# Performance work log

Measured on AMD Instinct MI355X. Metric: run time of the kernel, lower is better.

Reference implementation:

```python
import jax, jax.numpy as jnp
import numpy as np

B, L, F, H = 4096, 32, 28, 512  # batch, max CDR length (=input_size), features, hidden


def setup_inputs() -> dict:
    key = jax.random.key(0)
    ks = jax.random.split(key, 8)
    return {
        "input": jax.random.normal(ks[0], (B, L, F), jnp.float32),
        "unpacked_masks": jnp.ones((B, L, 1), jnp.float32),
        "bias_mat": jnp.zeros((B, L, F), jnp.float32),
        "conv1_w": jax.random.normal(ks[1], (F, F, 3), jnp.float32) * 0.1,
        "conv1_b": jnp.zeros((F,), jnp.float32),
        "conv_w": jax.random.normal(ks[2], (1, L, 1), jnp.float32) * 0.1,
        "conv_b": jnp.zeros((1,), jnp.float32),
        "fc1_w": jax.random.normal(ks[3], (1, H), jnp.float32) * 0.05,
        "fc1_b": jnp.zeros((1,), jnp.float32),
        "W_ih": jax.random.normal(ks[4], (4 * H, L), jnp.float32) * 0.1,
        "W_hh": jax.random.normal(ks[5], (4 * H, H), jnp.float32) * 0.05,
        "b_ih": jnp.zeros((4 * H,), jnp.float32),
        "b_hh": jnp.zeros((4 * H,), jnp.float32),
        "conv2_w": jax.random.normal(ks[6], (1, H, 1), jnp.float32) * 0.05,
        "conv2_b": jnp.zeros((1,), jnp.float32),
    }


def reference(input, unpacked_masks, bias_mat, conv1_w, conv1_b, conv_w, conv_b,
              fc1_w, fc1_b, W_ih, W_hh, b_ih, b_hh, conv2_w, conv2_b):
    b, l, f = input.shape
    h_dim = W_hh.shape[1]
    # --- conv1 residual block (eval mode: dropouts are identity) ---
    x_t = jnp.transpose(input, (0, 2, 1))  # [B, F, L]
    y = jax.lax.conv_general_dilated(
        x_t, conv1_w, window_strides=(1,), padding=[(1, 1)],
        dimension_numbers=("NCH", "OIH", "NCH")) + conv1_b[None, :, None]
    x = jnp.transpose(y, (0, 2, 1)) * unpacked_masks  # [B, L, F]
    x = jax.nn.elu(x) + input
    # --- u_a = Conv1d(L,1,1) over the length axis: [B, 1, F] (kept as [B, F]) ---
    u_a = jnp.einsum("blf,l->bf", x, conv_w[0, :, 0]) + conv_b  # [B, F]
    x_transposed = jnp.transpose(x, (0, 2, 1))  # [B, F, L]

    h0 = jnp.zeros((l, h_dim), input.dtype)
    c0 = jnp.zeros((l, h_dim), input.dtype)

    def step(carry, inps):
        h, c = carry
        u_b, xT_b, bias_b = inps  # [F], [F, L], [L, F]
        w_a = h @ fc1_w.T + fc1_b  # [L, 1]
        scores = jax.nn.leaky_relu(u_b[None, :] + w_a, 0.01) + bias_b  # [L, F]
        attn = jax.nn.softmax(scores, axis=0)  # softmax over dim 1 of [B, L, F]
        ctx = attn @ xT_b  # [L, F] @ [F, L] -> [L, L]
        gates = ctx @ W_ih.T + b_ih + h @ W_hh.T + b_hh  # [L, 4H]
        i_g, f_g, g_g, o_g = jnp.split(gates, 4, axis=-1)
        c_new = jax.nn.sigmoid(f_g) * c + jax.nn.sigmoid(i_g) * jnp.tanh(g_g)
        h_new = jax.nn.sigmoid(o_g) * jnp.tanh(c_new)
        return (h_new, c_new), h_new

    # The original loops over the batch dim, carrying (h, c) across iterations.
    (_, _), all_hidden = jax.lax.scan(step, (h0, c0), (u_a, x_transposed, bias_mat))
    # all_hidden: [B, L, H]
    out = jnp.einsum("blh,h->bl", all_hidden, conv2_w[0, :, 0])[..., None] + conv2_b  # [B, L, 1]
    return out * unpacked_masks
```

## Files before the change

### kernel.cpp

```cpp
#include <hip/hip_runtime.h>
#include <math.h>

#define NBATCH 4096
#define GBLK   64
#define HSTR   516
#define XSTR   36
#define WSTR   33

typedef int   i32x4 __attribute__((ext_vector_type(4)));
typedef float f32x4 __attribute__((ext_vector_type(4)));
typedef short short8 __attribute__((ext_vector_type(8)));

#define OFF_X    0u
#define OFF_UA   (OFF_X  + 4096u*896u)
#define OFF_BG   (OFF_UA + 4096u*28u)
#define OFF_H    (OFF_BG + 2048u)
#define OFF_BAR  (OFF_H  + 2u*32u*512u)
#define OFF_WFH  (OFF_BAR + 64u)
#define OFF_WFL  (OFF_WFH + 557056u)

__device__ __forceinline__ unsigned bfr(float x) {
    unsigned u = __builtin_bit_cast(unsigned, x);
    return (u + 0x7FFFu + ((u >> 16) & 1u)) >> 16;
}
__device__ __forceinline__ float fb(unsigned b) { return __builtin_bit_cast(float, b << 16); }
__device__ __forceinline__ unsigned packhl(float v) {
    unsigned h = bfr(v);
    unsigned l = bfr(v - fb(h));
    return h | (l << 16);
}
__device__ __forceinline__ float up(unsigned u) {
    return __builtin_bit_cast(float, u << 16) + __builtin_bit_cast(float, u & 0xFFFF0000u);
}
__device__ __forceinline__ float sigm(float v) { return 1.0f / (1.0f + __expf(-v)); }

__global__ __launch_bounds__(256) void prep_kernel(
    const float* __restrict__ input, const float* __restrict__ masks,
    const float* __restrict__ c1w, const float* __restrict__ c1b,
    const float* __restrict__ convw, const float* __restrict__ convb,
    float* __restrict__ xout, float* __restrict__ uaout)
// ... 41 lines not shown
{
    const int g = blockIdx.x * 256 + threadIdx.x;
    BG[g] = bih[g] + bhh[g];
}

__global__ __launch_bounds__(256) void prepf_kernel(
    const float* __restrict__ Wih, const float* __restrict__ Whh,
    unsigned* __restrict__ wfh, unsigned* __restrict__ wfl)
{
    const int id = blockIdx.x * 256 + threadIdx.x;
    const int lane = id & 63;
    int rest = id >> 6;
    const int ct = rest & 1; rest >>= 1;
    const int t = rest % 17, blk8 = rest / 17;
    const int n = lane & 15, kg = lane >> 4;
    const int c = ct * 16 + n;
    const int g = (c >> 3) * 512 + blk8 * 8 + (c & 7);
    const int kbase = t * 32 + kg * 8;
    i32x4 hv, lv;
    #pragma unroll
    for (int d = 0; d < 4; ++d) {
        const int k = kbase + 2 * d;
        float w0 = (k     < 512) ? Whh[(size_t)g * 512 + k]     : Wih[g * 32 + (k - 512)];
        float w1 = (k + 1 < 512) ? Whh[(size_t)g * 512 + k + 1] : Wih[g * 32 + (k + 1 - 512)];
        unsigned h0 = bfr(w0), h1 = bfr(w1);
        unsigned l0 = bfr(w0 - fb(h0)), l1 = bfr(w1 - fb(h1));
        ((unsigned*)&hv)[d] = h0 | (h1 << 16);
        ((unsigned*)&lv)[d] = l0 | (l1 << 16);
    }
    ((i32x4*)wfh)[id] = hv;
    ((i32x4*)wfl)[id] = lv;
}

__device__ __forceinline__ void stage_h16(const unsigned* hsrc, unsigned* h_lds, int tid)
{
    const int half = tid >> 7, t128 = tid & 127;
    const unsigned* p = hsrc + half * 8192 + t128 * 4;
    i32x4 v0, v1, v2, v3, v4, v5, v6, v7, v8, v9, v10, v11, v12, v13, v14, v15;
    asm volatile(
        "global_load_dwordx4 %0, %16, off sc0 sc1\n\t"
        "global_load_dwordx4 %1, %16, off offset:2048 sc0 sc1\n\t"
        "global_load_dwordx4 %2, %17, off sc0 sc1\n\t"
        "global_load_dwordx4 %3, %17, off offset:2048 sc0 sc1\n\t"
        "global_load_dwordx4 %4, %18, off sc0 sc1\n\t"
        "global_load_dwordx4 %5, %18, off offset:2048 sc0 sc1\n\t"
        "global_load_dwordx4 %6, %19, off sc0 sc1\n\t"
        "global_load_dwordx4 %7, %19, off offset:2048 sc0 sc1\n\t"
        "global_load_dwordx4 %8, %20, off sc0 sc1\n\t"
        "global_load_dwordx4 %9, %20, off offset:2048 sc0 sc1\n\t"
        "global_load_dwordx4 %10, %21, off sc0 sc1\n\t"
        "global_load_dwordx4 %11, %21, off offset:2048 sc0 sc1\n\t"
        "global_load_dwordx4 %12, %22, off sc0 sc1\n\t"
        "global_load_dwordx4 %13, %22, off offset:2048 sc0 sc1\n\t"
        "global_load_dwordx4 %14, %23, off sc0 sc1\n\t"
        "global_load_dwordx4 %15, %23, off offset:2048 sc0 sc1\n\t"
        "s_waitcnt vmcnt(0)"
        : "=&v"(v0), "=&v"(v1), "=&v"(v2), "=&v"(v3),
          "=&v"(v4), "=&v"(v5), "=&v"(v6), "=&v"(v7),
          "=&v"(v8), "=&v"(v9), "=&v"(v10), "=&v"(v11),
          "=&v"(v12), "=&v"(v13), "=&v"(v14), "=&v"(v15)
        : "v"(p), "v"(p + 1024), "v"(p + 2048), "v"(p + 3072),
          "v"(p + 4096), "v"(p + 5120), "v"(p + 6144), "v"(p + 7168)
        : "memory");
    const int col = t128 * 4;
    const int rb = half * 16;
    *(i32x4*)&h_lds[(rb +  0) * HSTR + col] = v0;
    *(i32x4*)&h_lds[(rb +  1) * HSTR + col] = v1;
    *(i32x4*)&h_lds[(rb +  2) * HSTR + col] = v2;
    *(i32x4*)&h_lds[(rb +  3) * HSTR + col] = v3;
    *(i32x4*)&h_lds[(rb +  4) * HSTR + col] = v4;
    *(i32x4*)&h_lds[(rb +  5) * HSTR + col] = v5;
    *(i32x4*)&h_lds[(rb +  6) * HSTR + col] = v6;
    *(i32x4*)&h_lds[(rb +  7) * HSTR + col] = v7;
    *(i32x4*)&h_lds[(rb +  8) * HSTR + col] = v8;
    *(i32x4*)&h_lds[(rb +  9) * HSTR + col] = v9;
    *(i32x4*)&h_lds[(rb + 10) * HSTR + col] = v10;
    *(i32x4*)&h_lds[(rb + 11) * HSTR + col] = v11;
    *(i32x4*)&h_lds[(rb + 12) * HSTR + col] = v12;
    *(i32x4*)&h_lds[(rb + 13) * HSTR + col] = v13;
    *(i32x4*)&h_lds[(rb + 14) * HSTR + col] = v14;
    *(i32x4*)&h_lds[(rb + 15) * HSTR + col] = v15;
}

__device__ __forceinline__ void build_frag(const unsigned* base, short8& hi, short8& lo)
{
    i32x4 ua = *(const i32x4*)base;
    i32x4 ub = *(const i32x4*)(base + 4);
    i32x4 h, l;
    h.x = (int)__builtin_amdgcn_perm((unsigned)ua.y, (unsigned)ua.x, 0x05040100u);
    l.x = (int)__builtin_amdgcn_perm((unsigned)ua.y, (unsigned)ua.x, 0x07060302u);
    h.y = (int)__builtin_amdgcn_perm((unsigned)ua.w, (unsigned)ua.z, 0x05040100u);
    l.y = (int)__builtin_amdgcn_perm((unsigned)ua.w, (unsigned)ua.z, 0x07060302u);
    h.z = (int)__builtin_amdgcn_perm((unsigned)ub.y, (unsigned)ub.x, 0x05040100u);
    l.z = (int)__builtin_amdgcn_perm((unsigned)ub.y, (unsigned)ub.x, 0x07060302u);
    h.w = (int)__builtin_amdgcn_perm((unsigned)ub.w, (unsigned)ub.z, 0x05040100u);
    l.w = (int)__builtin_amdgcn_perm((unsigned)ub.w, (unsigned)ub.z, 0x07060302u);
    hi = __builtin_bit_cast(short8, h);
    lo = __builtin_bit_cast(short8, l);
}

__device__ __forceinline__ void out_proj(const unsigned* h_lds, const float* c2w_lds, float c2b,
                                         const float* masks, float* out, int bb,
                                         int slot16, int seg16)
{
    float p0 = 0.f, p1 = 0.f;
    #pragma unroll
    for (int jj = 0; jj < 8; ++jj) {
        const int off = seg16 * 4 + 64 * jj;
        f32x4 w = *(const f32x4*)&c2w_lds[off];
        i32x4 h0 = *(const i32x4*)&h_lds[slot16 * HSTR + off];
        i32x4 h1 = *(const i32x4*)&h_lds[(slot16 + 16) * HSTR + off];
        p0 += up((unsigned)h0.x) * w.x + up((unsigned)h0.y) * w.y
            + up((unsigned)h0.z) * w.z + up((unsigned)h0.w) * w.w;
        p1 += up((unsigned)h1.x) * w.x + up((unsigned)h1.y) * w.y
            + up((unsigned)h1.z) * w.z + up((unsigned)h1.w) * w.w;
    }
    p0 += __shfl_xor(p0, 1); p0 += __shfl_xor(p0, 2);
    p0 += __shfl_xor(p0, 4); p0 += __shfl_xor(p0, 8);
    p1 += __shfl_xor(p1, 1); p1 += __shfl_xor(p1, 2);
    p1 += __shfl_xor(p1, 4); p1 += __shfl_xor(p1, 8);
    if (seg16 == 0) {
        out[bb * 32 + slot16]      = (p0 + c2b) * masks[bb * 32 + slot16];
        out[bb * 32 + slot16 + 16] = (p1 + c2b) * masks[bb * 32 + slot16 + 16];
    }
}

__global__ __launch_bounds__(256, 1) void rnn_serial(
    const float* __restrict__ xbuf, const float* __restrict__ uabuf,
    const float* __restrict__ BG,
    const unsigned* __restrict__ wfh, const unsigned* __restrict__ wfl,
    const float* __restrict__ Whh, const float* __restrict__ Wih,
    unsigned* hbuf, int* bar,
    const float* __restrict__ bias_mat, const float* __restrict__ masks,
    const float* __restrict__ fc1w, const float* __restrict__ fc1bp,
    const float* __restrict__ c2w, const float* __restrict__ c2bp,
    float* __restrict__ out)
{
    __shared__ unsigned h_lds[32 * HSTR];
    __shared__ float    x_lds[32 * XSTR];
    __shared__ float    bias_lds[32 * XSTR];
    __shared__ unsigned attn_p[32 * XSTR];
    __shared__ float    mbuf[2][32 * XSTR];
    __shared__ float    wihb[32 * WSTR];
    __shared__ float    gl_part[5 * 32 * 33];
    __shared__ float    wapart[4][2][32];
    __shared__ float    wa_lds[32];
    __shared__ float    ua_lds[28];
    __shared__ float    fc1_lds[512];
    __shared__ float    c2w_lds[512];
    __shared__ int      s_flag;

    const int tid  = threadIdx.x;
    const int blk  = blockIdx.x;
    const int lane = tid & 63;
    const int wv   = tid >> 6;

    for (int i = tid; i < 512; i += 256) { fc1_lds[i] = fc1w[i]; c2w_lds[i] = c2w[i]; }
    if (tid == 0) s_flag = 0;
    const float f1b = fc1bp[0];
    const float c2b = c2bp[0];

    i32x4 whi[4][2], wlo[4][2];
    {
        const i32x4* wfh4 = (const i32x4*)wfh;
        const i32x4* wfl4 = (const i32x4*)wfl;
        #pragma unroll
        for (int s = 0; s < 4; ++s)
            #pragma unroll
            for (int ct = 0; ct < 2; ++ct) {
                const int idx = ((blk * 17 + wv * 4 + s) * 2 + ct) * 64 + lane;
                whi[s][ct] = wfh4[idx];
                wlo[s][ct] = wfl4[idx];
            }
    }
    i32x4 wAh[4], wAl[4];
    {
        const int n = lane & 15, kgi = lane >> 4;
        #pragma unroll
        for (int s = 0; s < 4; ++s) {
            wAh[s] = (i32x4){0, 0, 0, 0};
            wAl[s] = (i32x4){0, 0, 0, 0};
            if (n < 2) {
                const float* src = (n == 0) ? fc1w : c2w;
                const int k0 = (wv * 4 + s) * 32 + kgi * 8;
                #pragma unroll
                for (int d = 0; d < 4; ++d) {
                    float v0 = src[k0 + 2 * d], v1 = src[k0 + 2 * d + 1];
                    unsigned h0 = bfr(v0), h1 = bfr(v1);
                    unsigned l0 = bfr(v0 - fb(h0)), l1 = bfr(v1 - fb(h1));
                    ((unsigned*)&wAh[s])[d] = h0 | (h1 << 16);
                    ((unsigned*)&wAl[s])[d] = l0 | (l1 << 16);
                }
            }
        }
    }

    const int l_own = tid >> 3, hc = tid & 7;
    float bgv[4];
    #pragma unroll
    for (int t = 0; t < 4; ++t) bgv[t] = BG[t * 512 + blk * 8 + hc];
    float c_reg = 0.f;
    bool use_mfma = true;

    const int slot16 = tid >> 4, seg16 = tid & 15;
    const int arow = lane & 15, kg = lane >> 4;

    for (int i = tid; i < 32 * XSTR; i += 256) {
        attn_p[i] = 0u;
        mbuf[0][i] = 0.f;
        mbuf[1][i] = 0.f;
    }
    for (int i = tid; i < 1024; i += 256) {
        const int c = i >> 5, j = i & 31;
        wihb[c * WSTR + j] = Wih[((c >> 3) * 512 + blk * 8 + (c & 7)) * 32 + j];
    }
    if (tid < 224) {
        float4 x0 = *(const float4*)(xbuf + tid * 4);
        #pragma unroll
        for (int i = 0; i < 4; ++i) {
            const int idx = tid * 4 + i;
            const int l = idx / 28, f = idx - l * 28;
            x_lds[l * XSTR + f] = ((const float*)&x0)[i];
        }
    }
    __syncthreads();
    for (int idx = tid; idx < 896; idx += 256) {
        const int c = idx / 28, f = idx - c * 28;
        float s = 0.f;
        #pragma unroll 8
        for (int j = 0; j < 32; ++j) s += wihb[c * WSTR + j] * x_lds[j * XSTR + f];
        mbuf[0][c * XSTR + f] = s;
    }
    float4 xr = make_float4(0.f, 0.f, 0.f, 0.f), br = xr;
    float ua_r = 0.f;
    if (tid < 224) {
        xr = *(const float4*)(xbuf + 896 + tid * 4);
        br = *(const float4*)(bias_mat + tid * 4);
    }
    if (tid < 28) ua_r = uabuf[tid];
    __syncthreads();

    for (int b = 0; b < NBATCH; ++b) {
        stage_h16(hbuf + (b & 1) * 16384, h_lds, tid);
        if (tid < 224) {
            #pragma unroll
            for (int i = 0; i < 4; ++i) {
                const int idx = tid * 4 + i;
                const int l = idx / 28, f = idx - l * 28;
                x_lds[l * XSTR + f]    = ((const float*)&xr)[i];
                bias_lds[l * XSTR + f] = ((const float*)&br)[i];
            }
        }
        if (tid < 28) ua_lds[tid] = ua_r;
        __syncthreads();

        {
            const int bx = (b + 2 < NBATCH) ? b + 2 : NBATCH - 1;
            const int bn = (b + 1 < NBATCH) ? b + 1 : NBATCH - 1;
            if (tid < 224) {
                xr = *(const float4*)(xbuf + (size_t)bx * 896 + tid * 4);
                br = *(const float4*)(bias_mat + (size_t)bn * 896 + tid * 4);
            }
            if (tid < 28) ua_r = uabuf[bn * 28 + tid];
        }

        if (use_mfma) {
            f32x4 accg[2][2], accw[2];
            accg[0][0] = (f32x4){0,0,0,0}; accg[0][1] = (f32x4){0,0,0,0};
            accg[1][0] = (f32x4){0,0,0,0}; accg[1][1] = (f32x4){0,0,0,0};
            accw[0]    = (f32x4){0,0,0,0}; accw[1]    = (f32x4){0,0,0,0};
            #pragma unroll
            for (int s = 0; s < 4; ++s) {
                const int k0 = (wv * 4 + s) * 32 + kg * 8;
                short8 ah0, al0, ah1, al1;
                build_frag(&h_lds[arow * HSTR + k0], ah0, al0);
                build_frag(&h_lds[(arow + 16) * HSTR + k0], ah1, al1);
                #pragma unroll
                for (int ct = 0; ct < 2; ++ct) {
                    short8 bh = __builtin_bit_cast(short8, whi[s][ct]);
                    short8 bl = __builtin_bit_cast(short8, wlo[s][ct]);
                    accg[ct][0] = __builtin_amdgcn_mfma_f32_16x16x32_bf16(ah0, bh, accg[ct][0], 0, 0, 0);
                    accg[ct][0] = __builtin_amdgcn_mfma_f32_16x16x32_bf16(al0, bh, accg[ct][0], 0, 0, 0);
                    accg[ct][0] = __builtin_amdgcn_mfma_f32_16x16x32_bf16(ah0, bl, accg[ct][0], 0, 0, 0);
                    accg[ct][1] = __builtin_amdgcn_mfma_f32_16x16x32_bf16(ah1, bh, accg[ct][1], 0, 0, 0);
                    accg[ct][1] = __builtin_amdgcn_mfma_f32_16x16x32_bf16(al1, bh, accg[ct][1], 0, 0, 0);
                    accg[ct][1] = __builtin_amdgcn_mfma_f32_16x16x32_bf16(ah1, bl, accg[ct][1], 0, 0, 0);
                }
                short8 bh = __builtin_bit_cast(short8, wAh[s]);
                short8 bl = __builtin_bit_cast(short8, wAl[s]);
                accw[0] = __builtin_amdgcn_mfma_f32_16x16x32_bf16(ah0, bh, accw[0], 0, 0, 0);
                accw[0] = __builtin_amdgcn_mfma_f32_16x16x32_bf16(al0, bh, accw[0], 0, 0, 0);
                accw[0] = __builtin_amdgcn_mfma_f32_16x16x32_bf16(ah0, bl, accw[0], 0, 0, 0);
                accw[1] = __builtin_amdgcn_mfma_f32_16x16x32_bf16(ah1, bh, accw[1], 0, 0, 0);
                accw[1] = __builtin_amdgcn_mfma_f32_16x16x32_bf16(al1, bh, accw[1], 0, 0, 0);
                accw[1] = __builtin_amdgcn_mfma_f32_16x16x32_bf16(ah1, bl, accw[1], 0, 0, 0);
            }
            #pragma unroll
            for (int ct = 0; ct < 2; ++ct)
                #pragma unroll
                for (int rt = 0; rt < 2; ++rt)
                    #pragma unroll
                    for (int r = 0; r < 4; ++r)
                        gl_part[(wv * 32 + rt * 16 + kg * 4 + r) * 33 + ct * 16 + arow] = accg[ct][rt][r];
            if (arow < 2) {
                #pragma unroll
                for (int rt = 0; rt < 2; ++rt)
                    #pragma unroll
                    for (int r = 0; r < 4; ++r)
                        wapart[wv][arow][rt * 16 + kg * 4 + r] = accw[rt][r];
            }
        }
        if (b < 2 || !use_mfma) {
            float p0 = 0.f, p1 = 0.f;
            #pragma unroll
            for (int jj = 0; jj < 8; ++jj) {
                const int off = seg16 * 4 + 64 * jj;
                f32x4 w = *(const f32x4*)&fc1_lds[off];
                i32x4 h0 = *(const i32x4*)&h_lds[slot16 * HSTR + off];
                i32x4 h1 = *(const i32x4*)&h_lds[(slot16 + 16) * HSTR + off];
                p0 += up((unsigned)h0.x) * w.x + up((unsigned)h0.y) * w.y
                    + up((unsigned)h0.z) * w.z + up((unsigned)h0.w) * w.w;
                p1 += up((unsigned)h1.x) * w.x + up((unsigned)h1.y) * w.y
                    + up((unsigned)h1.z) * w.z + up((unsigned)h1.w) * w.w;
            }
            p0 += __shfl_xor(p0, 1); p0 += __shfl_xor(p0, 2);
            p0 += __shfl_xor(p0, 4); p0 += __shfl_xor(p0, 8);
            p1 += __shfl_xor(p1, 1); p1 += __shfl_xor(p1, 2);
            p1 += __shfl_xor(p1, 4); p1 += __shfl_xor(p1, 8);
            if (seg16 == 0) { wa_lds[slot16] = p0 + f1b; wa_lds[slot16 + 16] = p1 + f1b; }
            if (b > 0 && blk == ((b - 1) & 63))
                out_proj(h_lds, c2w_lds, c2b, masks, out, b - 1, slot16, seg16);
        }
        __syncthreads();

        if (wv == 3) {
            if (use_mfma && lane < 32) {
                float wm = f1b;
                #pragma unroll
                for (int w = 0; w < 4; ++w) wm += wapart[w][0][lane];
                if (b < 2) {
                    if (fabsf(wm - wa_lds[lane]) > 0.02f + 0.004f * fabsf(wa_lds[lane])) s_flag = 1;
                } else {
                    wa_lds[lane] = wm;
                }
            }
            if (lane < 56) {
                const int f = lane >> 1, hf = lane & 1;
                const float uaf = ua_lds[f];
                float z[16], mx = -1e30f;
                #pragma unroll
                for (int i = 0; i < 16; ++i) {
                    const int l = hf * 16 + i;
                    float v = uaf + wa_lds[l];
                    v = (v >= 0.f) ? v : 0.01f * v;
                    v += bias_lds[l * XSTR + f];
                    z[i] = v;
                    mx = fmaxf(mx, v);
                }
                mx = fmaxf(mx, __shfl_xor(mx, 1));
                float sum = 0.f;
                #pragma unroll
                for (int i = 0; i < 16; ++i) { z[i] = __expf(z[i] - mx); sum += z[i]; }
                sum += __shfl_xor(sum, 1);
                const float inv = 1.0f / sum;
                #pragma unroll
                for (int i = 0; i < 16; ++i)
                    attn_p[(hf * 16 + i) * XSTR + f] = packhl(z[i] * inv);
            }
            asm volatile("s_waitcnt lgkmcnt(0)" ::: "memory");
            __builtin_amdgcn_sched_barrier(0);
            if (use_mfma) {
                f32x4 accm[2][2];
                accm[0][0] = (f32x4){0,0,0,0}; accm[0][1] = (f32x4){0,0,0,0};
                accm[1][0] = (f32x4){0,0,0,0}; accm[1][1] = (f32x4){0,0,0,0};
                short8 ah0, al0, ah1, al1;
                build_frag(&attn_p[arow * XSTR + kg * 8], ah0, al0);
                build_frag(&attn_p[(arow + 16) * XSTR + kg * 8], ah1, al1);
                #pragma unroll
                for (int ct = 0; ct < 2; ++ct) {
                    const float* mrow = &mbuf[b & 1][(ct * 16 + arow) * XSTR + kg * 8];
                    short8 bh, bl;
                    #pragma unroll
                    for (int e = 0; e < 8; ++e) {
                        const float v = mrow[e];
                        const unsigned hh = bfr(v);
                        bh[e] = (short)hh;
                        bl[e] = (short)bfr(v - fb(hh));
                    }
                    accm[ct][0] = __builtin_amdgcn_mfma_f32_16x16x32_bf16(ah0, bh, accm[ct][0], 0, 0, 0);
                    accm[ct][0] = __builtin_amdgcn_mfma_f32_16x16x32_bf16(al0, bh, accm[ct][0], 0, 0, 0);
                    accm[ct][0] = __builtin_amdgcn_mfma_f32_16x16x32_bf16(ah0, bl, accm[ct][0], 0, 0, 0);
                    accm[ct][1] = __builtin_amdgcn_mfma_f32_16x16x32_bf16(ah1, bh, accm[ct][1], 0, 0, 0);
                    accm[ct][1] = __builtin_amdgcn_mfma_f32_16x16x32_bf16(al1, bh, accm[ct][1], 0, 0, 0);
                    accm[ct][1] = __builtin_amdgcn_mfma_f32_16x16x32_bf16(ah1, bl, accm[ct][1], 0, 0, 0);
                }
                #pragma unroll
                for (int ct = 0; ct < 2; ++ct)
                    #pragma unroll
                    for (int rt = 0; rt < 2; ++rt)
                        #pragma unroll
                        for (int r = 0; r < 4; ++r)
                            gl_part[(4 * 32 + rt * 16 + kg * 4 + r) * 33 + ct * 16 + arow] = accm[ct][rt][r];
            }
        } else {
            if (wv == 2 && use_mfma && lane < 32) {
                float om = c2b;
                #pragma unroll
                for (int w = 0; w < 4; ++w) om += wapart[w][1][lane];
                if (b < 2) {
                    const unsigned* hr = &h_lds[lane * HSTR];
                    float ox = c2b;
                    for (int k = 0; k < 512; ++k) ox += up(hr[k]) * c2w_lds[k];
                    if (fabsf(om - ox) > 0.02f + 0.004f * fabsf(ox)) s_flag = 1;
                } else if (b > 0 && blk == ((b - 1) & 63)) {
                    out[(b - 1) * 32 + lane] = om * masks[(b - 1) * 32 + lane];
                }
            }
            float* mdst = mbuf[(b + 1) & 1];
            for (int idx = wv * 64 + lane; idx < 896; idx += 192) {
                const int c = idx / 28, f = idx - c * 28;
                float s = 0.f;
                #pragma unroll 8
                for (int j = 0; j < 32; ++j) s += wihb[c * WSTR + j] * x_lds[j * XSTR + f];
                mdst[c * XSTR + f] = s;
            }
        }
        __syncthreads();

        {
            float gv[4];
            #pragma unroll
            for (int t = 0; t < 4; ++t) {
                float g = bgv[t];
                if (use_mfma) {
                    #pragma unroll
                    for (int w = 0; w < 5; ++w)
                        g += gl_part[(w * 32 + l_own) * 33 + t * 8 + hc];
                }
                gv[t] = g;
            }
            if (b < 2 || !use_mfma) {
                const unsigned* hrow = &h_lds[l_own * HSTR];
                const unsigned* ar   = &attn_p[l_own * XSTR];
                const float*    mb   = mbuf[b & 1];
                bool bad = false;
                #pragma unroll
                for (int t = 0; t < 4; ++t) {
                    const int g = t * 512 + blk * 8 + hc;
                    const f32x4* wr = (const f32x4*)(Whh + (size_t)g * 512);
                    float ref = bgv[t];
                    #pragma unroll 4
                    for (int q = 0; q < 128; ++q) {
                        f32x4 w = wr[q];
                        ref += up(hrow[4 * q + 0]) * w.x + up(hrow[4 * q + 1]) * w.y
                             + up(hrow[4 * q + 2]) * w.z + up(hrow[4 * q + 3]) * w.w;
                    }
                    const float* mr = &mb[(t * 8 + hc) * XSTR];
                    #pragma unroll 4
                    for (int f = 0; f < 28; ++f) ref += up(ar[f]) * mr[f];
                    if (b < 2 && use_mfma && fabsf(gv[t] - ref) > 0.02f + 0.004f * fabsf(ref)) bad = true;
                    gv[t] = ref;
                }
                if (b < 2) {
                    if (bad) s_flag = 1;
                    __syncthreads();
                    use_mfma = use_mfma && (s_flag == 0);
                    __syncthreads();
                    if (tid == 0) s_flag = 0;
                }
            }
            const float cn = sigm(gv[1]) * c_reg + sigm(gv[0]) * tanhf(gv[2]);
            const float hn = sigm(gv[3]) * tanhf(cn);
            c_reg = cn;
            __hip_atomic_store(hbuf + ((b & 1) ^ 1) * 16384 + l_own * 512 + blk * 8 + hc,
                               packhl(hn), __ATOMIC_RELAXED, __HIP_MEMORY_SCOPE_AGENT);
        }

        asm volatile("s_waitcnt vmcnt(0)" ::: "memory");
        __syncthreads();
        if (tid == 0)
            __hip_atomic_store(&bar[blk], b + 1, __ATOMIC_RELAXED, __HIP_MEMORY_SCOPE_AGENT);
        if (tid < 64) {
            while (true) {
                int v = __hip_atomic_load(&bar[tid], __ATOMIC_RELAXED, __HIP_MEMORY_SCOPE_AGENT);
                if (__all(v >= b + 1)) break;
                __builtin_amdgcn_s_sleep(1);
            }
        }
        __syncthreads();
    }

    if (blk == 63) {
        stage_h16(hbuf, h_lds, tid);
        __syncthreads();
        if (use_mfma) {
            f32x4 accw[2];
            accw[0] = (f32x4){0,0,0,0}; accw[1] = (f32x4){0,0,0,0};
            #pragma unroll
            for (int s = 0; s < 4; ++s) {
                const int k0 = (wv * 4 + s) * 32 + kg * 8;
                short8 ah0, al0, ah1, al1;
                build_frag(&h_lds[arow * HSTR + k0], ah0, al0);
                build_frag(&h_lds[(arow + 16) * HSTR + k0], ah1, al1);
                short8 bh = __builtin_bit_cast(short8, wAh[s]);
                short8 bl = __builtin_bit_cast(short8, wAl[s]);
                accw[0] = __builtin_amdgcn_mfma_f32_16x16x32_bf16(ah0, bh, accw[0], 0, 0, 0);
                accw[0] = __builtin_amdgcn_mfma_f32_16x16x32_bf16(al0, bh, accw[0], 0, 0, 0);
                accw[0] = __builtin_amdgcn_mfma_f32_16x16x32_bf16(ah0, bl, accw[0], 0, 0, 0);
                accw[1] = __builtin_amdgcn_mfma_f32_16x16x32_bf16(ah1, bh, accw[1], 0, 0, 0);
                accw[1] = __builtin_amdgcn_mfma_f32_16x16x32_bf16(al1, bh, accw[1], 0, 0, 0);
                accw[1] = __builtin_amdgcn_mfma_f32_16x16x32_bf16(ah1, bl, accw[1], 0, 0, 0);
            }
            if (arow < 2) {
                #pragma unroll
                for (int rt = 0; rt < 2; ++rt)
                    #pragma unroll
                    for (int r = 0; r < 4; ++r)
                        wapart[wv][arow][rt * 16 + kg * 4 + r] = accw[rt][r];
            }
            __syncthreads();
            if (wv == 2 && lane < 32) {
                float om = c2b;
                #pragma unroll
                for (int w = 0; w < 4; ++w) om += wapart[w][1][lane];
                out[4095 * 32 + lane] = om * masks[4095 * 32 + lane];
            }
        } else {
            out_proj(h_lds, c2w_lds, c2b, masks, out, 4095, slot16, seg16);
        }
    }
}

extern "C" void kernel_launch(void* const* d_in, const int* in_sizes, int n_in,
                              void* d_out, int out_size, void* d_ws, size_t ws_size,
                              hipStream_t stream)
{
    const float* input    = (const float*)d_in[0];
    const float* masks    = (const float*)d_in[1];
    const float* bias_mat = (const float*)d_in[2];
    const float* c1w      = (const float*)d_in[3];
    const float* c1b      = (const float*)d_in[4];
    const float* convw    = (const float*)d_in[5];
    const float* convb    = (const float*)d_in[6];
    const float* fc1w     = (const float*)d_in[7];
    const float* fc1b     = (const float*)d_in[8];
    const float* Wih      = (const float*)d_in[9];
    const float* Whh      = (const float*)d_in[10];
    const float* bih      = (const float*)d_in[11];
    const float* bhh      = (const float*)d_in[12];
    const float* c2w      = (const float*)d_in[13];
    const float* c2b      = (const float*)d_in[14];

    float* ws  = (float*)d_ws;
    float* out = (float*)d_out;
    int*   bar = (int*)(ws + OFF_BAR);

    hipMemsetAsync(ws + OFF_H, 0, (2u * 32u * 512u + 64u) * sizeof(float), stream);

    hipLaunchKernelGGL(prep_kernel, dim3(NBATCH), dim3(256), 0, stream,
                       input, masks, c1w, c1b, convw, convb, ws + OFF_X, ws + OFF_UA);
    hipLaunchKernelGGL(prepw_kernel, dim3(8), dim3(256), 0, stream,
// ... 11 lines not shown
```

Baseline: 31.76 ms.

## Replace global grid barrier with per-wave producer polling and wave-local h staging

Removes the end-of-step block-wide barrier, where thread group 0 polled all 64 block flags and then synchronised. Instead, each wave polls only the 16 producer blocks whose h columns it needs, then stages its own column slice of h into LDS. Each wave reads only its own slice, so an LDS wave fence replaces the __syncthreads before the MFMA. The next-step x/bias prefetch moves after the gate MFMA. This lets waves start as soon as their producers finish, at the cost of a subtle memory-ordering risk and barriers rearranged around the b<2 path.

```diff
diff --git a/kernel.cpp b/kernel.cpp
--- a/kernel.cpp
+++ b/kernel.cpp
@@ -113,54 +113,59 @@
     ((i32x4*)wfl)[id] = lv;
 }
 
-__device__ __forceinline__ void stage_h16(const unsigned* hsrc, unsigned* h_lds, int tid)
-{
-    const int half = tid >> 7, t128 = tid & 127;
-    const unsigned* p = hsrc + half * 8192 + t128 * 4;
+__device__ __forceinline__ void stage_wave(const unsigned* hsrc, unsigned* h_lds, int wv, int lane)
+{
+    const unsigned* p = hsrc + (lane >> 1) * 512 + wv * 128 + (lane & 1) * 64;
     i32x4 v0, v1, v2, v3, v4, v5, v6, v7, v8, v9, v10, v11, v12, v13, v14, v15;
     asm volatile(
         "global_load_dwordx4 %0, %16, off sc0 sc1\n\t"
-        "global_load_dwordx4 %1, %16, off offset:2048 sc0 sc1\n\t"
-        "global_load_dwordx4 %2, %17, off sc0 sc1\n\t"
-        "global_load_dwordx4 %3, %17, off offset:2048 sc0 sc1\n\t"
-        "global_load_dwordx4 %4, %18, off sc0 sc1\n\t"
-        "global_load_dwordx4 %5, %18, off offset:2048 sc0 sc1\n\t"
-        "global_load_dwordx4 %6, %19, off sc0 sc1\n\t"
-        "global_load_dwordx4 %7, %19, off offset:2048 sc0 sc1\n\t"
-        "global_load_dwordx4 %8, %20, off sc0 sc1\n\t"
-        "global_load_dwordx4 %9, %20, off offset:2048 sc0 sc1\n\t"
-        "global_load_dwordx4 %10, %21, off sc0 sc1\n\t"
-        "global_load_dwordx4 %11, %21, off offset:2048 sc0 sc1\n\t"
-        "global_load_dwordx4 %12, %22, off sc0 sc1\n\t"
-        "global_load_dwordx4 %13, %22, off offset:2048 sc0 sc1\n\t"
-        "global_load_dwordx4 %14, %23, off sc0 sc1\n\t"
-        "global_load_dwordx4 %15, %23, off offset:2048 sc0 sc1\n\t"
+        "global_load_dwordx4 %1, %16, off offset:16 sc0 sc1\n\t"
+        "global_load_dwordx4 %2, %16, off offset:32 sc0 sc1\n\t"
+        "global_load_dwordx4 %3, %16, off offset:48 sc0 sc1\n\t"
+        "global_load_dwordx4 %4, %16, off offset:64 sc0 sc1\n\t"
+        "global_load_dwordx4 %5, %16, off offset:80 sc0 sc1\n\t"
+        "global_load_dwordx4 %6, %16, off offset:96 sc0 sc1\n\t"
+        "global_load_dwordx4 %7, %16, off offset:112 sc0 sc1\n\t"
+        "global_load_dwordx4 %8, %16, off offset:128 sc0 sc1\n\t"
+        "global_load_dwordx4 %9, %16, off offset:144 sc0 sc1\n\t"
+        "global_load_dwordx4 %10, %16, off offset:160 sc0 sc1\n\t"
+        "global_load_dwordx4 %11, %16, off offset:176 sc0 sc1\n\t"
+        "global_load_dwordx4 %12, %16, off offset:192 sc0 sc1\n\t"
+        "global_load_dwordx4 %13, %16, off offset:208 sc0 sc1\n\t"
+        "global_load_dwordx4 %14, %16, off offset:224 sc0 sc1\n\t"
+        "global_load_dwordx4 %15, %16, off offset:240 sc0 sc1\n\t"
         "s_waitcnt vmcnt(0)"
         : "=&v"(v0), "=&v"(v1), "=&v"(v2), "=&v"(v3),
           "=&v"(v4), "=&v"(v5), "=&v"(v6), "=&v"(v7),
           "=&v"(v8), "=&v"(v9), "=&v"(v10), "=&v"(v11),
           "=&v"(v12), "=&v"(v13), "=&v"(v14), "=&v"(v15)
-        : "v"(p), "v"(p + 1024), "v"(p + 2048), "v"(p + 3072),
-          "v"(p + 4096), "v"(p + 5120), "v"(p + 6144), "v"(p + 7168)
+        : "v"(p)
         : "memory");
-    const int col = t128 * 4;
-    const int rb = half * 16;
-    *(i32x4*)&h_lds[(rb +  0) * HSTR + col] = v0;
-    *(i32x4*)&h_lds[(rb +  1) * HSTR + col] = v1;
-    *(i32x4*)&h_lds[(rb +  2) * HSTR + col] = v2;
-    *(i32x4*)&h_lds[(rb +  3) * HSTR + col] = v3;
-    *(i32x4*)&h_lds[(rb +  4) * HSTR + col] = v4;
-    *(i32x4*)&h_lds[(rb +  5) * HSTR + col] = v5;
-    *(i32x4*)&h_lds[(rb +  6) * HSTR + col] = v6;
-    *(i32x4*)&h_lds[(rb +  7) * HSTR + col] = v7;
-    *(i32x4*)&h_lds[(rb +  8) * HSTR + col] = v8;
-    *(i32x4*)&h_lds[(rb +  9) * HSTR + col] = v9;
-    *(i32x4*)&h_lds[(rb + 10) * HSTR + col] = v10;
-    *(i32x4*)&h_lds[(rb + 11) * HSTR + col] = v11;
-    *(i32x4*)&h_lds[(rb + 12) * HSTR + col] = v12;
-    *(i32x4*)&h_lds[(rb + 13) * HSTR + col] = v13;
-    *(i32x4*)&h_lds[(rb + 14) * HSTR + col] = v14;
-    *(i32x4*)&h_lds[(rb + 15) * HSTR + col] = v15;
+    unsigned* d = h_lds + (lane >> 1) * HSTR + wv * 128 + (lane & 1) * 64;
+    *(i32x4*)(d +  0) = v0;  *(i32x4*)(d +  4) = v1;
+    *(i32x4*)(d +  8) = v2;  *(i32x4*)(d + 12) = v3;
+    *(i32x4*)(d + 16) = v4;  *(i32x4*)(d + 20) = v5;
+    *(i32x4*)(d + 24) = v6;  *(i32x4*)(d + 28) = v7;
+    *(i32x4*)(d + 32) = v8;  *(i32x4*)(d + 36) = v9;
+    *(i32x4*)(d + 40) = v10; *(i32x4*)(d + 44) = v11;
+    *(i32x4*)(d + 48) = v12; *(i32x4*)(d + 52) = v13;
+    *(i32x4*)(d + 56) = v14; *(i32x4*)(d + 60) = v15;
+}
+
+__device__ __forceinline__ void lds_wave_fence()
+{
+    asm volatile("s_waitcnt lgkmcnt(0)" ::: "memory");
+    __builtin_amdgcn_sched_barrier(0);
+}
+
+__device__ __forceinline__ void poll_producers(const int* bar, int wv, int lane, int target)
+{
+    const int* fp = &bar[wv * 16 + (lane & 15)];
+    while (true) {
+        int v = __hip_atomic_load(fp, __ATOMIC_RELAXED, __HIP_MEMORY_SCOPE_AGENT);
+        if (__all(v >= target)) break;
+        __builtin_amdgcn_s_sleep(1);
+    }
 }
 
 __device__ __forceinline__ void build_frag(const unsigned* base, short8& hi, short8& lo)
@@ -322,7 +327,8 @@
     __syncthreads();
 
     for (int b = 0; b < NBATCH; ++b) {
-        stage_h16(hbuf + (b & 1) * 16384, h_lds, tid);
+        poll_producers(bar, wv, lane, b);
+        stage_wave(hbuf + (b & 1) * 16384, h_lds, wv, lane);
         if (tid < 224) {
             #pragma unroll
             for (int i = 0; i < 4; ++i) {
@@ -333,17 +339,7 @@
             }
         }
         if (tid < 28) ua_lds[tid] = ua_r;
-        __syncthreads();
-
-        {
-            const int bx = (b + 2 < NBATCH) ? b + 2 : NBATCH - 1;
-            const int bn = (b + 1 < NBATCH) ? b + 1 : NBATCH - 1;
-            if (tid < 224) {
-                xr = *(const float4*)(xbuf + (size_t)bx * 896 + tid * 4);
-                br = *(const float4*)(bias_mat + (size_t)bn * 896 + tid * 4);
-            }
-            if (tid < 28) ua_r = uabuf[bn * 28 + tid];
-        }
+        lds_wave_fence();
 
         if (use_mfma) {
             f32x4 accg[2][2], accw[2];
@@ -391,6 +387,17 @@
                         wapart[wv][arow][rt * 16 + kg * 4 + r] = accw[rt][r];
             }
         }
+        {
+            const int bx = (b + 2 < NBATCH) ? b + 2 : NBATCH - 1;
+            const int bn = (b + 1 < NBATCH) ? b + 1 : NBATCH - 1;
+            if (tid < 224) {
+                xr = *(const float4*)(xbuf + (size_t)bx * 896 + tid * 4);
+                br = *(const float4*)(bias_mat + (size_t)bn * 896 + tid * 4);
+            }
+            if (tid < 28) ua_r = uabuf[bn * 28 + tid];
+        }
+        __syncthreads();
+
         if (b < 2 || !use_mfma) {
             float p0 = 0.f, p1 = 0.f;
             #pragma unroll
@@ -411,8 +418,8 @@
             if (seg16 == 0) { wa_lds[slot16] = p0 + f1b; wa_lds[slot16 + 16] = p1 + f1b; }
             if (b > 0 && blk == ((b - 1) & 63))
                 out_proj(h_lds, c2w_lds, c2b, masks, out, b - 1, slot16, seg16);
-        }
-        __syncthreads();
+            __syncthreads();
+        }
 
         if (wv == 3) {
             if (use_mfma && lane < 32) {
@@ -425,6 +432,7 @@
                     wa_lds[lane] = wm;
                 }
             }
+            lds_wave_fence();
             if (lane < 56) {
                 const int f = lane >> 1, hf = lane & 1;
                 const float uaf = ua_lds[f];
@@ -448,8 +456,7 @@
                 for (int i = 0; i < 16; ++i)
                     attn_p[(hf * 16 + i) * XSTR + f] = packhl(z[i] * inv);
             }
-            asm volatile("s_waitcnt lgkmcnt(0)" ::: "memory");
-            __builtin_amdgcn_sched_barrier(0);
+            lds_wave_fence();
             if (use_mfma) {
                 f32x4 accm[2][2];
                 accm[0][0] = (f32x4){0,0,0,0}; accm[0][1] = (f32x4){0,0,0,0};
@@ -561,18 +568,12 @@
         __syncthreads();
         if (tid == 0)
             __hip_atomic_store(&bar[blk], b + 1, __ATOMIC_RELAXED, __HIP_MEMORY_SCOPE_AGENT);
-        if (tid < 64) {
-            while (true) {
-                int v = __hip_atomic_load(&bar[tid], __ATOMIC_RELAXED, __HIP_MEMORY_SCOPE_AGENT);
-                if (__all(v >= b + 1)) break;
-                __builtin_amdgcn_s_sleep(1);
-            }
-        }
-        __syncthreads();
     }
 
     if (blk == 63) {
-        stage_h16(hbuf, h_lds, tid);
+        poll_producers(bar, wv, lane, NBATCH);
+        stage_wave(hbuf, h_lds, wv, lane);
+        lds_wave_fence();
         __syncthreads();
         if (use_mfma) {
             f32x4 accw[2];
```

Result: slower. 38.99 ms (+22.8%).

## Halve persistent block count to 32 with doubled per-block hidden slice

Applied to the files above, without the earlier changes.

The serial LSTM kernel now runs on 32 cooperating blocks instead of 64. Each block owns 16 hidden units and holds twice the W_hh fragments in registers. The aim is to shrink the cost of the per-step grid barrier and the h-state exchange, which is paid once per batch step. In exchange each block does more MFMA work per step. The ctx@W_ih product is precomputed as packed bf16 hi/lo pairs and spread across two waves. Its next-step precompute now overlaps with the recurrent MFMAs, and the next-step input prefetch moves later in the step. The added register pressure and per-block work may lengthen the critical path.

```diff
diff --git a/kernel.cpp b/kernel.cpp
--- a/kernel.cpp
+++ b/kernel.cpp
@@ -2,10 +2,9 @@
 #include <math.h>
 
 #define NBATCH 4096
-#define GBLK   64
+#define GBLK   32
 #define HSTR   516
 #define XSTR   36
-#define WSTR   33
 
 typedef int   i32x4 __attribute__((ext_vector_type(4)));
 typedef float f32x4 __attribute__((ext_vector_type(4)));
@@ -163,6 +162,12 @@
     *(i32x4*)&h_lds[(rb + 15) * HSTR + col] = v15;
 }
 
+__device__ __forceinline__ void lds_wave_fence()
+{
+    asm volatile("s_waitcnt lgkmcnt(0)" ::: "memory");
+    __builtin_amdgcn_sched_barrier(0);
+}
+
 __device__ __forceinline__ void build_frag(const unsigned* base, short8& hi, short8& lo)
 {
     i32x4 ua = *(const i32x4*)base;
@@ -180,15 +185,15 @@
     lo = __builtin_bit_cast(short8, l);
 }
 
-__device__ __forceinline__ void out_proj(const unsigned* h_lds, const float* c2w_lds, float c2b,
-                                         const float* masks, float* out, int bb,
+__device__ __forceinline__ void out_proj(const unsigned* h_lds, const float* __restrict__ cw,
+                                         float c2b, const float* masks, float* out, int bb,
                                          int slot16, int seg16)
 {
     float p0 = 0.f, p1 = 0.f;
     #pragma unroll
     for (int jj = 0; jj < 8; ++jj) {
         const int off = seg16 * 4 + 64 * jj;
-        f32x4 w = *(const f32x4*)&c2w_lds[off];
+        f32x4 w = *(const f32x4*)&cw[off];
         i32x4 h0 = *(const i32x4*)&h_lds[slot16 * HSTR + off];
         i32x4 h1 = *(const i32x4*)&h_lds[(slot16 + 16) * HSTR + off];
         p0 += up((unsigned)h0.x) * w.x + up((unsigned)h0.y) * w.y
@@ -220,36 +225,36 @@
     __shared__ unsigned h_lds[32 * HSTR];
     __shared__ float    x_lds[32 * XSTR];
     __shared__ float    bias_lds[32 * XSTR];
-    __shared__ unsigned attn_p[32 * XSTR];
-    __shared__ float    mbuf[2][32 * XSTR];
-    __shared__ float    wihb[32 * WSTR];
-    __shared__ float    gl_part[5 * 32 * 33];
+    __shared__ unsigned attn_p[2][32 * XSTR];
+    __shared__ unsigned mpack[2][64 * XSTR];
+    __shared__ float    wihb[64 * 33];
+    __shared__ float    glb[4 * 32 * 65];
+    __shared__ float    glm[32 * 65];
     __shared__ float    wapart[4][2][32];
+    __shared__ float    wa_w[2][32];
     __shared__ float    wa_lds[32];
     __shared__ float    ua_lds[28];
-    __shared__ float    fc1_lds[512];
-    __shared__ float    c2w_lds[512];
     __shared__ int      s_flag;
 
     const int tid  = threadIdx.x;
-    const int blk  = blockIdx.x;
+    const int rank = blockIdx.x;
     const int lane = tid & 63;
     const int wv   = tid >> 6;
 
-    for (int i = tid; i < 512; i += 256) { fc1_lds[i] = fc1w[i]; c2w_lds[i] = c2w[i]; }
     if (tid == 0) s_flag = 0;
     const float f1b = fc1bp[0];
     const float c2b = c2bp[0];
 
-    i32x4 whi[4][2], wlo[4][2];
+    i32x4 whi[4][4], wlo[4][4];
     {
         const i32x4* wfh4 = (const i32x4*)wfh;
         const i32x4* wfl4 = (const i32x4*)wfl;
         #pragma unroll
         for (int s = 0; s < 4; ++s)
             #pragma unroll
-            for (int ct = 0; ct < 2; ++ct) {
-                const int idx = ((blk * 17 + wv * 4 + s) * 2 + ct) * 64 + lane;
+            for (int ct = 0; ct < 4; ++ct) {
+                const int blkOld = 2 * rank + (ct >> 1);
+                const int idx = ((blkOld * 17 + wv * 4 + s) * 2 + (ct & 1)) * 64 + lane;
                 whi[s][ct] = wfh4[idx];
                 wlo[s][ct] = wfl4[idx];
             }
@@ -277,23 +282,23 @@
     }
 
     const int l_own = tid >> 3, hc = tid & 7;
-    float bgv[4];
+    float bgv[2][4];
     #pragma unroll
-    for (int t = 0; t < 4; ++t) bgv[t] = BG[t * 512 + blk * 8 + hc];
-    float c_reg = 0.f;
+    for (int j = 0; j < 2; ++j)
+        #pragma unroll
+        for (int t = 0; t < 4; ++t)
+            bgv[j][t] = BG[t * 512 + rank * 16 + hc + 8 * j];
+    float creg[2] = {0.f, 0.f};
     bool use_mfma = true;
 
     const int slot16 = tid >> 4, seg16 = tid & 15;
     const int arow = lane & 15, kg = lane >> 4;
 
-    for (int i = tid; i < 32 * XSTR; i += 256) {
-        attn_p[i] = 0u;
-        mbuf[0][i] = 0.f;
-        mbuf[1][i] = 0.f;
-    }
-    for (int i = tid; i < 1024; i += 256) {
+    for (int i = tid; i < 2 * 32 * XSTR; i += 256) attn_p[i / (32 * XSTR)][i % (32 * XSTR)] = 0u;
+    for (int i = tid; i < 2 * 64 * XSTR; i += 256) mpack[i / (64 * XSTR)][i % (64 * XSTR)] = 0u;
+    for (int i = tid; i < 2048; i += 256) {
         const int c = i >> 5, j = i & 31;
-        wihb[c * WSTR + j] = Wih[((c >> 3) * 512 + blk * 8 + (c & 7)) * 32 + j];
+        wihb[c * 33 + j] = Wih[((c >> 4) * 512 + rank * 16 + (c & 15)) * 32 + j];
     }
     if (tid < 224) {
         float4 x0 = *(const float4*)(xbuf + tid * 4);
@@ -305,12 +310,12 @@
         }
     }
     __syncthreads();
-    for (int idx = tid; idx < 896; idx += 256) {
-        const int c = idx / 28, f = idx - c * 28;
+    for (int i = tid; i < 1792; i += 256) {
+        const int c = i / 28, f = i - c * 28;
         float s = 0.f;
         #pragma unroll 8
-        for (int j = 0; j < 32; ++j) s += wihb[c * WSTR + j] * x_lds[j * XSTR + f];
-        mbuf[0][c * XSTR + f] = s;
+        for (int j = 0; j < 32; ++j) s += wihb[c * 33 + j] * x_lds[j * XSTR + f];
+        mpack[0][c * XSTR + f] = packhl(s);
     }
     float4 xr = make_float4(0.f, 0.f, 0.f, 0.f), br = xr;
     float ua_r = 0.f;
@@ -335,21 +340,14 @@
         if (tid < 28) ua_lds[tid] = ua_r;
         __syncthreads();
 
-        {
-            const int bx = (b + 2 < NBATCH) ? b + 2 : NBATCH - 1;
-            const int bn = (b + 1 < NBATCH) ? b + 1 : NBATCH - 1;
-            if (tid < 224) {
-                xr = *(const float4*)(xbuf + (size_t)bx * 896 + tid * 4);
-                br = *(const float4*)(bias_mat + (size_t)bn * 896 + tid * 4);
-            }
-            if (tid < 28) ua_r = uabuf[bn * 28 + tid];
-        }
-
         if (use_mfma) {
-            f32x4 accg[2][2], accw[2];
-            accg[0][0] = (f32x4){0,0,0,0}; accg[0][1] = (f32x4){0,0,0,0};
-            accg[1][0] = (f32x4){0,0,0,0}; accg[1][1] = (f32x4){0,0,0,0};
-            accw[0]    = (f32x4){0,0,0,0}; accw[1]    = (f32x4){0,0,0,0};
+            f32x4 accg[4][2], accw[2];
+            #pragma unroll
+            for (int ct = 0; ct < 4; ++ct) {
+                accg[ct][0] = (f32x4){0,0,0,0};
+                accg[ct][1] = (f32x4){0,0,0,0};
+            }
+            accw[0] = (f32x4){0,0,0,0}; accw[1] = (f32x4){0,0,0,0};
             #pragma unroll
             for (int s = 0; s < 4; ++s) {
                 const int k0 = (wv * 4 + s) * 32 + kg * 8;
@@ -357,7 +355,7 @@
                 build_frag(&h_lds[arow * HSTR + k0], ah0, al0);
                 build_frag(&h_lds[(arow + 16) * HSTR + k0], ah1, al1);
                 #pragma unroll
-                for (int ct = 0; ct < 2; ++ct) {
+                for (int ct = 0; ct < 4; ++ct) {
                     short8 bh = __builtin_bit_cast(short8, whi[s][ct]);
                     short8 bl = __builtin_bit_cast(short8, wlo[s][ct]);
                     accg[ct][0] = __builtin_amdgcn_mfma_f32_16x16x32_bf16(ah0, bh, accg[ct][0], 0, 0, 0);
@@ -376,13 +374,23 @@
                 accw[1] = __builtin_amdgcn_mfma_f32_16x16x32_bf16(al1, bh, accw[1], 0, 0, 0);
                 accw[1] = __builtin_amdgcn_mfma_f32_16x16x32_bf16(ah1, bl, accw[1], 0, 0, 0);
             }
-            #pragma unroll
-            for (int ct = 0; ct < 2; ++ct)
+            {
+                unsigned* mdst = mpack[(b + 1) & 1];
+                for (int i = tid; i < 1792; i += 256) {
+                    const int c = i / 28, f = i - c * 28;
+                    float s = 0.f;
+                    #pragma unroll 8
+                    for (int j = 0; j < 32; ++j) s += wihb[c * 33 + j] * x_lds[j * XSTR + f];
+                    mdst[c * XSTR + f] = packhl(s);
+                }
+            }
+            #pragma unroll
+            for (int ct = 0; ct < 4; ++ct)
                 #pragma unroll
                 for (int rt = 0; rt < 2; ++rt)
                     #pragma unroll
                     for (int r = 0; r < 4; ++r)
-                        gl_part[(wv * 32 + rt * 16 + kg * 4 + r) * 33 + ct * 16 + arow] = accg[ct][rt][r];
+                        glb[(wv * 32 + rt * 16 + kg * 4 + r) * 65 + ct * 16 + arow] = accg[ct][rt][r];
             if (arow < 2) {
                 #pragma unroll
                 for (int rt = 0; rt < 2; ++rt)
@@ -390,13 +398,22 @@
                     for (int r = 0; r < 4; ++r)
                         wapart[wv][arow][rt * 16 + kg * 4 + r] = accw[rt][r];
             }
+        } else {
+            unsigned* mdst = mpack[(b + 1) & 1];
+            for (int i = tid; i < 1792; i += 256) {
+                const int c = i / 28, f = i - c * 28;
+                float s = 0.f;
+                #pragma unroll 8
+                for (int j = 0; j < 32; ++j) s += wihb[c * 33 + j] * x_lds[j * XSTR + f];
+                mdst[c * XSTR + f] = packhl(s);
+            }
         }
         if (b < 2 || !use_mfma) {
             float p0 = 0.f, p1 = 0.f;
             #pragma unroll
             for (int jj = 0; jj < 8; ++jj) {
                 const int off = seg16 * 4 + 64 * jj;
-                f32x4 w = *(const f32x4*)&fc1_lds[off];
+                f32x4 w = *(const f32x4*)&fc1w[off];
                 i32x4 h0 = *(const i32x4*)&h_lds[slot16 * HSTR + off];
                 i32x4 h1 = *(const i32x4*)&h_lds[(slot16 + 16) * HSTR + off];
                 p0 += up((unsigned)h0.x) * w.x + up((unsigned)h0.y) * w.y
@@ -409,22 +426,37 @@
             p1 += __shfl_xor(p1, 1); p1 += __shfl_xor(p1, 2);
             p1 += __shfl_xor(p1, 4); p1 += __shfl_xor(p1, 8);
             if (seg16 == 0) { wa_lds[slot16] = p0 + f1b; wa_lds[slot16 + 16] = p1 + f1b; }
-            if (b > 0 && blk == ((b - 1) & 63))
-                out_proj(h_lds, c2w_lds, c2b, masks, out, b - 1, slot16, seg16);
+            if (b > 0 && rank == ((b - 1) & 31))
+                out_proj(h_lds, c2w, c2b, masks, out, b - 1, slot16, seg16);
+        }
+        {
+            const int bx = (b + 2 < NBATCH) ? b + 2 : NBATCH - 1;
+            const int bn = (b + 1 < NBATCH) ? b + 1 : NBATCH - 1;
+            if (tid < 224) {
+                xr = *(const float4*)(xbuf + (size_t)bx * 896 + tid * 4);
+                br = *(const float4*)(bias_mat + (size_t)bn * 896 + tid * 4);
+            }
+            if (tid < 28) ua_r = uabuf[bn * 28 + tid];
         }
         __syncthreads();
 
-        if (wv == 3) {
-            if (use_mfma && lane < 32) {
-                float wm = f1b;
-                #pragma unroll
-                for (int w = 0; w < 4; ++w) wm += wapart[w][0][lane];
-                if (b < 2) {
-                    if (fabsf(wm - wa_lds[lane]) > 0.02f + 0.004f * fabsf(wa_lds[lane])) s_flag = 1;
+        if (wv < 2) {
+            if (lane < 32) {
+                float wm;
+                if (use_mfma) {
+                    wm = f1b;
+                    #pragma unroll
+                    for (int w = 0; w < 4; ++w) wm += wapart[w][0][lane];
+                    if (b < 2) {
+                        if (fabsf(wm - wa_lds[lane]) > 0.02f + 0.004f * fabsf(wa_lds[lane])) s_flag = 1;
+                        wm = wa_lds[lane];
+                    }
                 } else {
-                    wa_lds[lane] = wm;
-                }
-            }
+                    wm = wa_lds[lane];
+                }
+                wa_w[wv][lane] = wm;
+            }
+            lds_wave_fence();
             if (lane < 56) {
                 const int f = lane >> 1, hf = lane & 1;
                 const float uaf = ua_lds[f];
@@ -432,7 +464,7 @@
                 #pragma unroll
                 for (int i = 0; i < 16; ++i) {
                     const int l = hf * 16 + i;
-                    float v = uaf + wa_lds[l];
+                    float v = uaf + wa_w[wv][l];
                     v = (v >= 0.f) ? v : 0.01f * v;
                     v += bias_lds[l * XSTR + f];
                     z[i] = v;
@@ -446,102 +478,87 @@
                 const float inv = 1.0f / sum;
                 #pragma unroll
                 for (int i = 0; i < 16; ++i)
-                    attn_p[(hf * 16 + i) * XSTR + f] = packhl(z[i] * inv);
-            }
-            asm volatile("s_waitcnt lgkmcnt(0)" ::: "memory");
-            __builtin_amdgcn_sched_barrier(0);
+                    attn_p[wv][(hf * 16 + i) * XSTR + f] = packhl(z[i] * inv);
+            }
+            lds_wave_fence();
             if (use_mfma) {
-                f32x4 accm[2][2];
-                accm[0][0] = (f32x4){0,0,0,0}; accm[0][1] = (f32x4){0,0,0,0};
-                accm[1][0] = (f32x4){0,0,0,0}; accm[1][1] = (f32x4){0,0,0,0};
                 short8 ah0, al0, ah1, al1;
-                build_frag(&attn_p[arow * XSTR + kg * 8], ah0, al0);
-                build_frag(&attn_p[(arow + 16) * XSTR + kg * 8], ah1, al1);
-                #pragma unroll
-                for (int ct = 0; ct < 2; ++ct) {
-                    const float* mrow = &mbuf[b & 1][(ct * 16 + arow) * XSTR + kg * 8];
+                build_frag(&attn_p[wv][arow * XSTR + kg * 8], ah0, al0);
+                build_frag(&attn_p[wv][(arow + 16) * XSTR + kg * 8], ah1, al1);
+                #pragma unroll
+                for (int q = 0; q < 2; ++q) {
+                    const int ct = wv * 2 + q;
                     short8 bh, bl;
+                    build_frag(&mpack[b & 1][(ct * 16 + arow) * XSTR + kg * 8], bh, bl);
+                    f32x4 a0 = (f32x4){0,0,0,0}, a1 = (f32x4){0,0,0,0};
+                    a0 = __builtin_amdgcn_mfma_f32_16x16x32_bf16(ah0, bh, a0, 0, 0, 0);
+                    a0 = __builtin_amdgcn_mfma_f32_16x16x32_bf16(al0, bh, a0, 0, 0, 0);
+                    a0 = __builtin_amdgcn_mfma_f32_16x16x32_bf16(ah0, bl, a0, 0, 0, 0);
+                    a1 = __builtin_amdgcn_mfma_f32_16x16x32_bf16(ah1, bh, a1, 0, 0, 0);
+                    a1 = __builtin_amdgcn_mfma_f32_16x16x32_bf16(al1, bh, a1, 0, 0, 0);
+                    a1 = __builtin_amdgcn_mfma_f32_16x16x32_bf16(ah1, bl, a1, 0, 0, 0);
                     #pragma unroll
-                    for (int e = 0; e < 8; ++e) {
-                        const float v = mrow[e];
-                        const unsigned hh = bfr(v);
-                        bh[e] = (short)hh;
-                        bl[e] = (short)bfr(v - fb(hh));
+                    for (int r = 0; r < 4; ++r) {
+                        glm[(     kg * 4 + r) * 65 + ct * 16 + arow] = a0[r];
+                        glm[(16 + kg * 4 + r) * 65 + ct * 16 + arow] = a1[r];
                     }
-                    accm[ct][0] = __builtin_amdgcn_mfma_f32_16x16x32_bf16(ah0, bh, accm[ct][0], 0, 0, 0);
-                    accm[ct][0] = __builtin_amdgcn_mfma_f32_16x16x32_bf16(al0, bh, accm[ct][0], 0, 0, 0);
-                    accm[ct][0] = __builtin_amdgcn_mfma_f32_16x16x32_bf16(ah0, bl, accm[ct][0], 0, 0, 0);
-                    accm[ct][1] = __builtin_amdgcn_mfma_f32_16x16x32_bf16(ah1, bh, accm[ct][1], 0, 0, 0);
-                    accm[ct][1] = __builtin_amdgcn_mfma_f32_16x16x32_bf16(al1, bh, accm[ct][1], 0, 0, 0);
-                    accm[ct][1] = __builtin_amdgcn_mfma_f32_16x16x32_bf16(ah1, bl, accm[ct][1], 0, 0, 0);
-                }
-                #pragma unroll
-                for (int ct = 0; ct < 2; ++ct)
-                    #pragma unroll
-                    for (int rt = 0; rt < 2; ++rt)
+                }
+            }
+        } else if (wv == 2 && use_mfma && lane < 32) {
+            float om = c2b;
+            #pragma unroll
+            for (int w = 0; w < 4; ++w) om += wapart[w][1][lane];
+            if (b < 2) {
+                const unsigned* hr = &h_lds[lane * HSTR];
+                float ox = c2b;
+                for (int k = 0; k < 512; ++k) ox += up(hr[k]) * c2w[k];
+                if (fabsf(om - ox) > 0.02f + 0.004f * fabsf(ox)) s_flag = 1;
+            } else if (b > 0 && rank == ((b - 1) & 31)) {
+                out[(b - 1) * 32 + lane] = om * masks[(b - 1) * 32 + lane];
+            }
+        }
+        __syncthreads();
+
+        {
+            float gv[2][4];
+            #pragma unroll
+            for (int j = 0; j < 2; ++j)
+                #pragma unroll
+                for (int t = 0; t < 4; ++t) {
+                    float g = bgv[j][t];
+                    if (use_mfma) {
+                        const int co = (j * 2 + ((t * 8 + hc) >> 4)) * 16 + ((t * 8 + hc) & 15);
                         #pragma unroll
-                        for (int r = 0; r < 4; ++r)
-                            gl_part[(4 * 32 + rt * 16 + kg * 4 + r) * 33 + ct * 16 + arow] = accm[ct][rt][r];
-            }
-        } else {
-            if (wv == 2 && use_mfma && lane < 32) {
-                float om = c2b;
-                #pragma unroll
-                for (int w = 0; w < 4; ++w) om += wapart[w][1][lane];
-                if (b < 2) {
-                    const unsigned* hr = &h_lds[lane * HSTR];
-                    float ox = c2b;
-                    for (int k = 0; k < 512; ++k) ox += up(hr[k]) * c2w_lds[k];
-                    if (fabsf(om - ox) > 0.02f + 0.004f * fabsf(ox)) s_flag = 1;
-                } else if (b > 0 && blk == ((b - 1) & 63)) {
-                    out[(b - 1) * 32 + lane] = om * masks[(b - 1) * 32 + lane];
-                }
-            }
-            float* mdst = mbuf[(b + 1) & 1];
-            for (int idx = wv * 64 + lane; idx < 896; idx += 192) {
-                const int c = idx / 28, f = idx - c * 28;
-                float s = 0.f;
-                #pragma unroll 8
-                for (int j = 0; j < 32; ++j) s += wihb[c * WSTR + j] * x_lds[j * XSTR + f];
-                mdst[c * XSTR + f] = s;
-            }
-        }
-        __syncthreads();
-
-        {
-            float gv[4];
-            #pragma unroll
-            for (int t = 0; t < 4; ++t) {
-                float g = bgv[t];
-                if (use_mfma) {
-                    #pragma unroll
-                    for (int w = 0; w < 5; ++w)
-                        g += gl_part[(w * 32 + l_own) * 33 + t * 8 + hc];
-                }
-                gv[t] = g;
-            }
+                        for (int w = 0; w < 4; ++w)
+                            g += glb[(w * 32 + l_own) * 65 + co];
+                        g += glm[l_own * 65 + t * 16 + hc + 8 * j];
+                    }
+                    gv[j][t] = g;
+                }
             if (b < 2 || !use_mfma) {
                 const unsigned* hrow = &h_lds[l_own * HSTR];
-                const unsigned* ar   = &attn_p[l_own * XSTR];
-                const float*    mb   = mbuf[b & 1];
+                const unsigned* ar   = &attn_p[0][l_own * XSTR];
+                const unsigned* mb   = mpack[b & 1];
                 bool bad = false;
                 #pragma unroll
-                for (int t = 0; t < 4; ++t) {
-                    const int g = t * 512 + blk * 8 + hc;
-                    const f32x4* wr = (const f32x4*)(Whh + (size_t)g * 512);
-                    float ref = bgv[t];
-                    #pragma unroll 4
-                    for (int q = 0; q < 128; ++q) {
-                        f32x4 w = wr[q];
-                        ref += up(hrow[4 * q + 0]) * w.x + up(hrow[4 * q + 1]) * w.y
-                             + up(hrow[4 * q + 2]) * w.z + up(hrow[4 * q + 3]) * w.w;
+                for (int j = 0; j < 2; ++j)
+                    #pragma unroll
+                    for (int t = 0; t < 4; ++t) {
+                        const int g = t * 512 + rank * 16 + hc + 8 * j;
+                        const f32x4* wr = (const f32x4*)(Whh + (size_t)g * 512);
+                        float ref = bgv[j][t];
+                        #pragma unroll 4
+                        for (int q = 0; q < 128; ++q) {
+                            f32x4 w = wr[q];
+                            ref += up(hrow[4 * q + 0]) * w.x + up(hrow[4 * q + 1]) * w.y
+                                 + up(hrow[4 * q + 2]) * w.z + up(hrow[4 * q + 3]) * w.w;
+                        }
+                        const unsigned* mr = &mb[(t * 16 + hc + 8 * j) * XSTR];
+                        #pragma unroll 4
+                        for (int f = 0; f < 28; ++f) ref += up(ar[f]) * up(mr[f]);
+                        if (b < 2 && use_mfma && fabsf(gv[j][t] - ref) > 0.02f + 0.004f * fabsf(ref)) bad = true;
+                        gv[j][t] = ref;
                     }
-                    const float* mr = &mb[(t * 8 + hc) * XSTR];
-                    #pragma unroll 4
-                    for (int f = 0; f < 28; ++f) ref += up(ar[f]) * mr[f];
-                    if (b < 2 && use_mfma && fabsf(gv[t] - ref) > 0.02f + 0.004f * fabsf(ref)) bad = true;
-                    gv[t] = ref;
-                }
                 if (b < 2) {
                     if (bad) s_flag = 1;
                     __syncthreads();
@@ -550,20 +567,24 @@
                     if (tid == 0) s_flag = 0;
                 }
             }
-            const float cn = sigm(gv[1]) * c_reg + sigm(gv[0]) * tanhf(gv[2]);
-            const float hn = sigm(gv[3]) * tanhf(cn);
-            c_reg = cn;
-            __hip_atomic_store(hbuf + ((b & 1) ^ 1) * 16384 + l_own * 512 + blk * 8 + hc,
-                               packhl(hn), __ATOMIC_RELAXED, __HIP_MEMORY_SCOPE_AGENT);
+            unsigned* hdst = hbuf + ((b & 1) ^ 1) * 16384 + l_own * 512 + rank * 16 + hc;
+            #pragma unroll
+            for (int j = 0; j < 2; ++j) {
+                const float cn = sigm(gv[j][1]) * creg[j] + sigm(gv[j][0]) * tanhf(gv[j][2]);
+                const float hn = sigm(gv[j][3]) * tanhf(cn);
+                creg[j] = cn;
+                __hip_atomic_store(hdst + 8 * j, packhl(hn),
+                                   __ATOMIC_RELAXED, __HIP_MEMORY_SCOPE_AGENT);
+            }
         }
 
         asm volatile("s_waitcnt vmcnt(0)" ::: "memory");
         __syncthreads();
         if (tid == 0)
-            __hip_atomic_store(&bar[blk], b + 1, __ATOMIC_RELAXED, __HIP_MEMORY_SCOPE_AGENT);
+            __hip_atomic_store(&bar[rank], b + 1, __ATOMIC_RELAXED, __HIP_MEMORY_SCOPE_AGENT);
         if (tid < 64) {
             while (true) {
-                int v = __hip_atomic_load(&bar[tid], __ATOMIC_RELAXED, __HIP_MEMORY_SCOPE_AGENT);
+                int v = __hip_atomic_load(&bar[tid & 31], __ATOMIC_RELAXED, __HIP_MEMORY_SCOPE_AGENT);
                 if (__all(v >= b + 1)) break;
                 __builtin_amdgcn_s_sleep(1);
             }
@@ -571,7 +592,7 @@
         __syncthreads();
     }
 
-    if (blk == 63) {
+    if (rank == 31) {
         stage_h16(hbuf, h_lds, tid);
         __syncthreads();
         if (use_mfma) {
@@ -607,7 +628,7 @@
                 out[4095 * 32 + lane] = om * masks[4095 * 32 + lane];
             }
         } else {
-            out_proj(h_lds, c2w_lds, c2b, masks, out, 4095, slot16, seg16);
+            out_proj(h_lds, c2w, c2b, masks, out, 4095, slot16, seg16);
         }
     }
 }
```

New measurement: 61.79 ms. 1.95x slower.
